# Optimization experiments

Measured on AMD Instinct MI355X. Metric: run time of the kernel, lower is better.

The kernel has to match this reference:

```python
import jax, jax.numpy as jnp
from jax import lax
import numpy as np

VOCAB, TAGS, EMB, HID = 50000, 45, 256, 512
B, S = 32, 256


def setup_inputs() -> dict:
    key = jax.random.key(0)
    ks = jax.random.split(key, 12)
    sc = 0.05
    return {
        "x": jax.random.randint(ks[0], (B, S), 0, VOCAB),
        "tags": jax.random.randint(ks[1], (B, S), 0, TAGS),
        "emb": jax.random.normal(ks[2], (VOCAB, EMB), jnp.float32) * sc,
        "w_ih_f": jax.random.normal(ks[3], (4 * HID, EMB), jnp.float32) * sc,
        "w_hh_f": jax.random.normal(ks[4], (4 * HID, HID), jnp.float32) * sc,
        "b_f": jnp.zeros((4 * HID,), jnp.float32),
        "w_ih_b": jax.random.normal(ks[5], (4 * HID, EMB), jnp.float32) * sc,
        "w_hh_b": jax.random.normal(ks[6], (4 * HID, HID), jnp.float32) * sc,
        "b_b": jnp.zeros((4 * HID,), jnp.float32),
        "lin_w": jax.random.normal(ks[7], (TAGS, 2 * HID), jnp.float32) * sc,
        "lin_b": jnp.zeros((TAGS,), jnp.float32),
        "start_t": jax.random.normal(ks[8], (TAGS,), jnp.float32) * 0.1,
        "end_t": jax.random.normal(ks[9], (TAGS,), jnp.float32) * 0.1,
        "trans": jax.random.normal(ks[10], (TAGS,), jnp.float32)[:, None] * 0.0 + jax.random.normal(ks[11], (TAGS, TAGS), jnp.float32) * 0.1,
    }


def _lstm_dir(xs, w_ih, w_hh, b, reverse):
    # xs: [B,S,E]. PyTorch gate order: i, f, g, o.
    Bsz = xs.shape[0]
    H = w_hh.shape[1]
    def step(carry, x_t):
        h, c = carry
        g = x_t @ w_ih.T + h @ w_hh.T + b
        i, f, gg, o = jnp.split(g, 4, axis=-1)
        c = jax.nn.sigmoid(f) * c + jax.nn.sigmoid(i) * jnp.tanh(gg)
        h = jax.nn.sigmoid(o) * jnp.tanh(c)
        return (h, c), h
    init = (jnp.zeros((Bsz, H), xs.dtype), jnp.zeros((Bsz, H), xs.dtype))
    _, hs = lax.scan(step, init, jnp.swapaxes(xs, 0, 1), reverse=reverse)
    return jnp.swapaxes(hs, 0, 1)  # [B,S,H]


def _crf_nll(em, tags, start_t, end_t, trans):
    # em: [B,S,T]; numerator: score of gold path
    em_sc = jnp.take_along_axis(em, tags[..., None], axis=2)[..., 0].sum(axis=1)
    tr_sc = trans[tags[:, :-1], tags[:, 1:]].sum(axis=1)
    score = start_t[tags[:, 0]] + em_sc + tr_sc + end_t[tags[:, -1]]
    # partition function via forward algorithm (logsumexp recurrence)
    alpha0 = start_t + em[:, 0]  # [B,T]
    def step(alpha, e_t):
        alpha = jax.nn.logsumexp(alpha[:, :, None] + trans[None], axis=1) + e_t
        return alpha, None
    alpha, _ = lax.scan(step, alpha0, jnp.swapaxes(em[:, 1:], 0, 1))
    logZ = jax.nn.logsumexp(alpha + end_t, axis=1)
    return -(score - logZ).mean()  # reduction='mean', loss = -llh


def reference(x, tags, emb, w_ih_f, w_hh_f, b_f, w_ih_b, w_hh_b, b_b,
              lin_w, lin_b, start_t, end_t, trans):
    embeds = emb[x]                               # [B,S,E]
    h_f = _lstm_dir(embeds, w_ih_f, w_hh_f, b_f, False)
    h_b = _lstm_dir(embeds, w_ih_b, w_hh_b, b_b, True)
    lstm_out = jnp.concatenate([h_f, h_b], axis=-1)  # [B,S,2H]
    emissions = lstm_out @ lin_w.T + lin_b           # [B,S,T]
    return _crf_nll(emissions, tags, start_t, end_t, trans)
```

## Files before the change

kernel.cpp:

```cpp
#include <hip/hip_runtime.h>

#define BB 32
#define SS 256
#define EMBD 256
#define HIDD 512
#define NTAG 45
#define TPAD 48
#define NBLK 32
#define ROWS 64
#define APAD 520
#define GRID_REC 256

typedef __bf16 bf16x8 __attribute__((ext_vector_type(8)));
typedef float  f32x4  __attribute__((ext_vector_type(4)));
typedef short  s16x8  __attribute__((ext_vector_type(8)));

__device__ __forceinline__ unsigned short f2bf(float x) {
  unsigned u = __builtin_bit_cast(unsigned, x);
  u = (u + 0x7fffu + ((u >> 16) & 1u)) >> 16;
  return (unsigned short)u;
}
__device__ __forceinline__ float bf2f(unsigned short u) {
  unsigned v = ((unsigned)u) << 16; return __builtin_bit_cast(float, v);
}

__device__ __forceinline__ unsigned ld32_cpol(const unsigned* p, bool sys) {
  unsigned v;
  if (sys) asm volatile("global_load_dword %0, %1, off sc0 sc1\ns_waitcnt vmcnt(0)"
                        : "=v"(v) : "v"(p) : "memory");
  else     asm volatile("global_load_dword %0, %1, off sc0\ns_waitcnt vmcnt(0)"
                        : "=v"(v) : "v"(p) : "memory");
  return v;
}
__device__ __forceinline__ void st32_cpol(unsigned* p, unsigned v, bool sys) {
  if (sys) asm volatile("global_store_dword %0, %1, off sc0 sc1" :: "v"(p), "v"(v) : "memory");
  else     asm volatile("global_store_dword %0, %1, off sc0"     :: "v"(p), "v"(v) : "memory");
}

#define LD8(CPOL)                                                           \
  asm volatile("global_load_dwordx4 %0, %[q0], off " CPOL "\n\t"            \
               "global_load_dwordx4 %1, %[q1], off " CPOL "\n\t"            \
               "global_load_dwordx4 %2, %[q2], off " CPOL "\n\t"            \
               "global_load_dwordx4 %3, %[q3], off " CPOL "\n\t"            \
               "global_load_dwordx4 %4, %[q4], off " CPOL "\n\t"            \
               "global_load_dwordx4 %5, %[q5], off " CPOL "\n\t"            \
               "global_load_dwordx4 %6, %[q6], off " CPOL "\n\t"            \
               "global_load_dwordx4 %7, %[q7], off " CPOL "\n\t"            \
               "s_waitcnt vmcnt(0)"                                         \
               : "=&v"(v0), "=&v"(v1), "=&v"(v2), "=&v"(v3),                \
                 "=&v"(v4), "=&v"(v5), "=&v"(v6), "=&v"(v7)                 \
               : [q0] "v"(p), [q1] "v"(p + 2048), [q2] "v"(p + 4096),       \
                 [q3] "v"(p + 6144), [q4] "v"(p + 8192), [q5] "v"(p + 10240),\
                 [q6] "v"(p + 12288), [q7] "v"(p + 14336)                   \
               : "memory")

__global__ void k_pack_e(const int* __restrict__ x, const float* __restrict__ emb,
                         unsigned short* __restrict__ E) {
  int idx = blockIdx.x * 256 + threadIdx.x;
  int e = idx & 255; int bt = idx >> 8; int b = bt & 31; int t = bt >> 5;
  int tok = x[b * SS + t];
  E[idx] = f2bf(emb[(long)tok * EMBD + e]);
}

__global__ void k_pack_w(const float* __restrict__ wih_f, const float* __restrict__ whh_f,
                         const float* __restrict__ bf_,  const float* __restrict__ wih_b,
                         const float* __restrict__ whh_b, const float* __restrict__ bb_,
                         unsigned short* __restrict__ Wh, unsigned short* __restrict__ Wie,
                         float* __restrict__ Bh) {
  long idx = (long)blockIdx.x * 256 + threadIdx.x;
  int k = (int)(idx % 768); long rest = idx / 768;
  int r2 = (int)(rest & 2047); int dir = (int)(rest >> 11);
  int blk = r2 >> 6, rl = r2 & 63, gate = rl >> 4, hl = rl & 15;
  int orig = gate * HIDD + blk * 16 + hl;
  const float* wih = dir ? wih_b : wih_f;
  const float* whh = dir ? whh_b : whh_f;
  if (k < HIDD) Wh[((long)(dir * 2048 + r2)) * 512 + k] = f2bf(whh[(long)orig * HIDD + k]);
  else          Wie[((long)(dir * 2048 + r2)) * 256 + (k - 512)] = f2bf(wih[(long)orig * EMBD + (k - 512)]);
  if (k == 0) {
    const float* bias = dir ? bb_ : bf_;
    Bh[dir * 2048 + r2] = bias[orig];
  }
}

__global__ void k_pack_l(const float* __restrict__ lin_w, const float* __restrict__ lin_b,
                         unsigned short* __restrict__ LW, float* __restrict__ LB) {
  int idx = blockIdx.x * 256 + threadIdx.x;
  if (idx < TPAD * 1024) {
    int tag = idx >> 10; int c = idx & 1023;
    LW[idx] = (tag < NTAG) ? f2bf(lin_w[tag * 1024 + c]) : (unsigned short)0;
  } else if (idx < TPAD * 1024 + TPAD) {
    int tag = idx - TPAD * 1024;
    LB[tag] = (tag < NTAG) ? lin_b[tag] : 0.f;
  }
}

__launch_bounds__(256)
__global__ void k_eproj(const unsigned short* __restrict__ E,
                        const unsigned short* __restrict__ Wie,
                        const float* __restrict__ Bh,
                        unsigned short* __restrict__ Ep) {
  __shared__ unsigned short W2[64 * 264];
  const int bx = blockIdx.x;
  const int tg = bx & 63, blk = (bx >> 6) & 31, dir = bx >> 11;
  const int tid = threadIdx.x;
  const int w = tid >> 6, lane = tid & 63;
  const int lm = lane & 15, quad = lane >> 4;

  {
    const unsigned short* src = Wie + ((long)(dir * 2048 + blk * 64)) * 256;
    for (int i = 0; i < 8; ++i) {
      int c = i * 256 + tid;
      int row = c >> 5, off = c & 31;
      *(s16x8*)&W2[row * 264 + off * 8] = *(const s16x8*)&src[row * 256 + off * 8];
    }
  }
  __syncthreads();

  f32x4 acc[2][4] = {};
#pragma unroll
  for (int kk = 0; kk < 8; ++kk) {
    s16x8 av[2];
#pragma unroll
    for (int sub = 0; sub < 2; ++sub)
      av[sub] = *(const s16x8*)&E[((long)(tg * 128 + w * 32 + sub * 16 + lm)) * 256 + kk * 32 + quad * 8];
#pragma unroll
    for (int sub = 0; sub < 2; ++sub)
#pragma unroll
      for (int n = 0; n < 4; ++n) {
        s16x8 bs = *(const s16x8*)&W2[(n * 16 + lm) * 264 + kk * 32 + quad * 8];
        acc[sub][n] = __builtin_amdgcn_mfma_f32_16x16x32_bf16(
            __builtin_bit_cast(bf16x8, av[sub]), __builtin_bit_cast(bf16x8, bs), acc[sub][n], 0, 0, 0);
      }
  }
  float bh[4];
#pragma unroll
  for (int n = 0; n < 4; ++n) bh[n] = Bh[dir * 2048 + blk * 64 + n * 16 + lm];
#pragma unroll
  for (int sub = 0; sub < 2; ++sub)
#pragma unroll
    for (int n = 0; n < 4; ++n)
#pragma unroll
      for (int r = 0; r < 4; ++r) {
        int m = w * 32 + sub * 16 + quad * 4 + r;
        int t = tg * 4 + (m >> 5), b = m & 31;
        int row_l = n * 16 + lm;
        Ep[((((long)(dir * 32 + blk) * 256 + t) * 32 + b) * 64) + row_l] =
            f2bf(acc[sub][n][r] + bh[n]);
      }
}

__launch_bounds__(256, 1)
__global__ void k_rec(const unsigned short* __restrict__ Wh,
                      const unsigned short* __restrict__ Ep,
                      unsigned short* __restrict__ H,
                      unsigned int* __restrict__ sync) {
  __shared__ unsigned short A_ls[32 * APAD];
  __shared__ float G_ls[32 * 66 + 4608];
  __shared__ int fast_ls;

  const int bx = blockIdx.x;
  const int role = bx & 7;
  if (role >= 2) return;
  const int dir = role;
  const int blk = bx >> 3;
  const int tid = threadIdx.x;
  const int w = tid >> 6, lane = tid & 63;
  const int lm = lane & 15, quad = lane >> 4;
  const int mt = w >> 1, nt = w & 1;

  unsigned int* det   = sync;
  unsigned int* flags = sync + 64;

  s16x8 wb[2][16];
  {
    const unsigned short* wsrc =
        Wh + ((long)(dir * 2048 + blk * 64 + nt * 32 + lm)) * 512 + quad * 8;
#pragma unroll
    for (int ns = 0; ns < 2; ++ns)
#pragma unroll
      for (int kk = 0; kk < 16; ++kk)
        wb[ns][kk] = *(const s16x8*)&wsrc[ns * 16 * 512 + kk * 32];
  }

  unsigned xcc;
  asm volatile("s_getreg_b32 %0, hwreg(HW_REG_XCC_ID)" : "=s"(xcc));
  if (tid == 0) st32_cpol(&det[dir * 32 + blk], xcc | 0x100u, true);
  if (w == 0) {
    unsigned v;
    for (;;) {
      v = (lane < 32) ? ld32_cpol(&det[dir * 32 + lane], true) : (xcc | 0x100u);
      if (__ballot(v != 0u) == ~0ull) break;
      __builtin_amdgcn_s_sleep(1);
    }
    if (lane == 0) fast_ls = (__ballot(v == (xcc | 0x100u)) == ~0ull) ? 1 : 0;
  }
  __syncthreads();
  const bool fast = (fast_ls != 0);
  __threadfence();

  const int gb = tid >> 3, hp = tid & 7;
  float c0 = 0.f, c1 = 0.f;

  unsigned short* Hd = H + (long)dir * SS * BB * HIDD;
  unsigned int* flagd = flags + dir * SS * NBLK;
  const unsigned short* Epd = Ep + ((long)(dir * 32 + blk) * 256) * 32 * 64;

  for (int t = 0; t < SS; ++t) {
    const int tE = (dir == 0) ? t : (SS - 1 - t);

    unsigned short epv[8];
    {
      const unsigned short* eb =
          Epd + ((long)tE * 32 + (mt * 16 + quad * 4)) * 64 + nt * 32 + lm;
#pragma unroll
      for (int ns = 0; ns < 2; ++ns)
#pragma unroll
        for (int r = 0; r < 4; ++r) epv[ns * 4 + r] = eb[r * 64 + ns * 16];
    }

    f32x4 acc0 = {0.f, 0.f, 0.f, 0.f}, acc1 = {0.f, 0.f, 0.f, 0.f};
    if (t > 0) {
      if (w == 0) {
        const unsigned int* fl = flagd + (long)(t - 1) * NBLK;
        for (;;) {
          unsigned f = (lane < 32) ? ld32_cpol(&fl[lane], !fast) : 1u;
          if (__ballot(f != 0u) == ~0ull) break;
          __builtin_amdgcn_s_sleep(1);
        }
      }
      __syncthreads();
      {
        const int hslot = (dir == 0) ? (t - 1) : (SS - t);
        const unsigned short* p = Hd + (long)hslot * BB * HIDD + w * 512 + lane * 8;
        s16x8 v0, v1, v2, v3, v4, v5, v6, v7;
        if (fast) { LD8("sc0"); } else { LD8("sc0 sc1"); }
        unsigned short* d = &A_ls[w * APAD + lane * 8];
        *(s16x8*)(d + 0 * 2080) = v0; *(s16x8*)(d + 1 * 2080) = v1;
        *(s16x8*)(d + 2 * 2080) = v2; *(s16x8*)(d + 3 * 2080) = v3;
        *(s16x8*)(d + 4 * 2080) = v4; *(s16x8*)(d + 5 * 2080) = v5;
        *(s16x8*)(d + 6 * 2080) = v6; *(s16x8*)(d + 7 * 2080) = v7;
      }
      __syncthreads();
#pragma unroll
      for (int kk = 0; kk < 16; ++kk) {
        s16x8 av = *(const s16x8*)&A_ls[(mt * 16 + lm) * APAD + kk * 32 + quad * 8];
        acc0 = __builtin_amdgcn_mfma_f32_16x16x32_bf16(
            __builtin_bit_cast(bf16x8, av), __builtin_bit_cast(bf16x8, wb[0][kk]), acc0, 0, 0, 0);
        acc1 = __builtin_amdgcn_mfma_f32_16x16x32_bf16(
            __builtin_bit_cast(bf16x8, av), __builtin_bit_cast(bf16x8, wb[1][kk]), acc1, 0, 0, 0);
      }
    }
#pragma unroll
    for (int r = 0; r < 4; ++r) {
      int mm = mt * 16 + quad * 4 + r;
      G_ls[mm * 66 + nt * 32 + lm]      = acc0[r] + bf2f(epv[r]);
      G_ls[mm * 66 + nt * 32 + 16 + lm] = acc1[r] + bf2f(epv[4 + r]);
    }
    __syncthreads();
    {
      float gi0 = G_ls[gb * 66 + 0  + 2 * hp], gi1 = G_ls[gb * 66 + 0  + 2 * hp + 1];
      float gf0 = G_ls[gb * 66 + 16 + 2 * hp], gf1 = G_ls[gb * 66 + 16 + 2 * hp + 1];
      float gg0 = G_ls[gb * 66 + 32 + 2 * hp], gg1 = G_ls[gb * 66 + 32 + 2 * hp + 1];
      float go0 = G_ls[gb * 66 + 48 + 2 * hp], go1 = G_ls[gb * 66 + 48 + 2 * hp + 1];
      float si0 = 1.f / (1.f + __expf(-gi0)), si1 = 1.f / (1.f + __expf(-gi1));
      float sf0 = 1.f / (1.f + __expf(-gf0)), sf1 = 1.f / (1.f + __expf(-gf1));
      float so0 = 1.f / (1.f + __expf(-go0)), so1 = 1.f / (1.f + __expf(-go1));
      float tg0 = tanhf(gg0), tg1 = tanhf(gg1);
      c0 = sf0 * c0 + si0 * tg0;
      c1 = sf1 * c1 + si1 * tg1;
      float h0 = so0 * tanhf(c0), h1 = so1 * tanhf(c1);
      int tslot = (dir == 0) ? t : (SS - 1 - t);
      unsigned hv = (unsigned)f2bf(h0) | ((unsigned)f2bf(h1) << 16);
      st32_cpol((unsigned*)&Hd[(long)tslot * BB * HIDD + (long)gb * HIDD + blk * 16 + 2 * hp],
                hv, !fast);
    }
    __syncthreads();
    if (t < SS - 1 && tid == 0)
      st32_cpol(&flagd[(long)t * NBLK + blk], 1u, !fast);
  }
}

__launch_bounds__(256)
__global__ void k_emis(const unsigned short* __restrict__ H,
                       const unsigned short* __restrict__ LW,
                       const float* __restrict__ LB,
                       float* __restrict__ EM) {
  const int row0 = blockIdx.x * 32;
  const int tid = threadIdx.x;
  const int w = tid >> 6, lane = tid & 63;
  const int lm = lane & 15, quad = lane >> 4;
  const unsigned short* Hf = H;
  const unsigned short* Hb = H + (long)SS * BB * HIDD;

  for (int tile = w; tile < 6; tile += 4) {
    int mt = tile / 3, nt = tile % 3;
    int arow = row0 + mt * 16 + lm;
    int nrow = nt * 16 + lm;
    f32x4 acc = {0.f, 0.f, 0.f, 0.f};
#pragma unroll 4
    for (int kk = 0; kk < 32; ++kk) {
      int k0 = kk * 32 + quad * 8;
      s16x8 asv = (k0 < HIDD) ? *(const s16x8*)&Hf[(long)arow * HIDD + k0]
                              : *(const s16x8*)&Hb[(long)arow * HIDD + (k0 - HIDD)];
      s16x8 bsv = *(const s16x8*)&LW[nrow * 1024 + k0];
      acc = __builtin_amdgcn_mfma_f32_16x16x32_bf16(
          __builtin_bit_cast(bf16x8, asv), __builtin_bit_cast(bf16x8, bsv), acc, 0, 0, 0);
    }
    float bias = LB[nrow];
#pragma unroll
    for (int r = 0; r < 4; ++r) {
      int mm = row0 + mt * 16 + quad * 4 + r;
      EM[(long)mm * TPAD + nrow] = acc[r] + bias;
    }
  }
}

__global__ void k_crf(const int* __restrict__ tags, const float* __restrict__ start_t,
                      const float* __restrict__ end_t, const float* __restrict__ trans,
                      const float* __restrict__ EM, float* __restrict__ chain) {
  __shared__ float T_ls[NTAG * TPAD];
  __shared__ float ET[48 * 48 + 16];
  __shared__ float P_ls[64];
  const int b = blockIdx.x;
  const int lane = threadIdx.x;
  const int j = lane;

  for (int i = lane; i < NTAG * NTAG; i += 64)
    T_ls[(i / NTAG) * TPAD + (i % NTAG)] = trans[i];
  for (int i = lane; i < 48 * 48 + 16; i += 64) ET[i] = 0.f;
  __syncthreads();

  float Mj = -1e30f;
  if (j < NTAG) {
    for (int i = 0; i < NTAG; ++i) Mj = fmaxf(Mj, T_ls[i * TPAD + j]);
    for (int i = 0; i < NTAG; ++i) ET[i * 48 + j] = __expf(T_ls[i * TPAD + j] - Mj);
  }
  __syncthreads();

  float et[48];
#pragma unroll
  for (int i = 0; i < 48; ++i) et[i] = ET[i * 48 + j];

  float part = 0.f;
  for (int t = lane; t < SS; t += 64) {
    int tg = tags[b * SS + t];
    part += EM[((long)t * BB + b) * TPAD + tg];
    if (t + 1 < SS) part += T_ls[tg * TPAD + tags[b * SS + t + 1]];
    if (t == 0)      part += start_t[tg];
    if (t == SS - 1) part += end_t[tg];
  }
  for (int off = 32; off; off >>= 1) part += __shfl_down(part, off);
  float score = __shfl(part, 0);

  float alpha = (j < NTAG) ? (start_t[j] + EM[(long)b * TPAD + j]) : -1e30f;
  float e_next = (j < NTAG) ? EM[((long)BB + b) * TPAD + j] : 0.f;
  for (int t = 1; t < SS; ++t) {
    float e_cur = e_next;
    if (t < SS - 1) e_next = (j < NTAG) ? EM[((long)(t + 1) * BB + b) * TPAD + j] : 0.f;
    float am = alpha;
#pragma unroll
    for (int off = 32; off; off >>= 1) am = fmaxf(am, __shfl_xor(am, off));
    float p = __expf(alpha - am);
    P_ls[lane] = p;
    __builtin_amdgcn_wave_barrier();
    float s0 = 0.f, s1 = 0.f, s2 = 0.f, s3 = 0.f;
#pragma unroll
    for (int i0 = 0; i0 < 48; i0 += 4) {
      f32x4 pv = *(const f32x4*)&P_ls[i0];
      s0 += pv.x * et[i0];
      s1 += pv.y * et[i0 + 1];
      s2 += pv.z * et[i0 + 2];
      s3 += pv.w * et[i0 + 3];
    }
    __builtin_amdgcn_wave_barrier();
    float s = (s0 + s1) + (s2 + s3);
    float na = am + Mj + __logf(s) + e_cur;
    alpha = (j < NTAG) ? na : -1e30f;
  }
  float v = (j < NTAG) ? (alpha + end_t[j]) : -1e30f;
  float mx = v;
  for (int off = 32; off; off >>= 1) mx = fmaxf(mx, __shfl_xor(mx, off));
  float s = __expf(v - mx);
  for (int off = 32; off; off >>= 1) s += __shfl_xor(s, off);
  if (lane == 0) chain[b] = score - (mx + __logf(s));
}

__global__ void k_fin(const float* __restrict__ chain, float* __restrict__ out) {
  int lane = threadIdx.x;
  float v = (lane < BB) ? chain[lane] : 0.f;
  for (int off = 32; off; off >>= 1) v += __shfl_xor(v, off);
  if (lane == 0) out[0] = -v / (float)BB;
}

extern "C" void kernel_launch(void* const* d_in, const int* in_sizes, int n_in,
                              void* d_out, int out_size, void* d_ws, size_t ws_size,
                              hipStream_t stream) {
  const int*   x      = (const int*)d_in[0];
  const int*   tags   = (const int*)d_in[1];
  const float* emb    = (const float*)d_in[2];
  const float* wih_f  = (const float*)d_in[3];
  const float* whh_f  = (const float*)d_in[4];
  const float* b_f    = (const float*)d_in[5];
  const float* wih_b  = (const float*)d_in[6];
  const float* whh_b  = (const float*)d_in[7];
  const float* b_b    = (const float*)d_in[8];
  const float* lin_w  = (const float*)d_in[9];
  const float* lin_b  = (const float*)d_in[10];
  const float* start_t= (const float*)d_in[11];
  const float* end_t  = (const float*)d_in[12];
  const float* trans  = (const float*)d_in[13];

  char* ws = (char*)d_ws;
  size_t off = 0;
  auto alloc = [&](size_t bytes) {
    void* p = ws + off; off = (off + bytes + 255) & ~(size_t)255; return p;
  };
  size_t sync_bytes = (64 + 2 * SS * NBLK) * 4;
  unsigned int*   sync = (unsigned int*) alloc(sync_bytes);
  unsigned short* E   = (unsigned short*)alloc((size_t)SS * BB * EMBD * 2);
  unsigned short* Wh  = (unsigned short*)alloc((size_t)2 * 2048 * 512 * 2);
  unsigned short* Wie = (unsigned short*)alloc((size_t)2 * 2048 * 256 * 2);
  float*          Bh  = (float*)         alloc((size_t)2 * 2048 * 4);
  unsigned short* Ep  = (unsigned short*)alloc((size_t)2 * 32 * 256 * 32 * 64 * 2);
  unsigned short* H   = (unsigned short*)alloc((size_t)2 * SS * BB * HIDD * 2);
  unsigned short* LW  = (unsigned short*)alloc((size_t)TPAD * 1024 * 2);
  float*          LB  = (float*)         alloc((size_t)TPAD * 4);
  float*          EM  = (float*)         alloc((size_t)SS * BB * TPAD * 4);
  float*          chain = (float*)       alloc((size_t)BB * 4);

  hipMemsetAsync(sync, 0, sync_bytes, stream);
  k_pack_e<<<dim3((SS * BB * EMBD) / 256), dim3(256), 0, stream>>>(x, emb, E);
  k_pack_w<<<dim3((2 * 2048 * 768) / 256), dim3(256), 0, stream>>>(
      wih_f, whh_f, b_f, wih_b, whh_b, b_b, Wh, Wie, Bh);
  k_pack_l<<<dim3((TPAD * 1024 + TPAD + 255) / 256), dim3(256), 0, stream>>>(
      lin_w, lin_b, LW, LB);
  k_eproj<<<dim3(4096), dim3(256), 0, stream>>>(E, Wie, Bh, Ep);

  void* kargs[] = {&Wh, &Ep, &H, &sync};
  hipLaunchCooperativeKernel((const void*)k_rec, dim3(GRID_REC), dim3(256), kargs, 0, stream);

  k_emis<<<dim3((SS * BB) / 32), dim3(256), 0, stream>>>(H, LW, LB, EM);
  k_crf<<<dim3(BB), dim3(64), 0, stream>>>(tags, start_t, end_t, trans, EM, chain);
  k_fin<<<dim3(1), dim3(64), 0, stream>>>(chain, (float*)d_out);
}
```

Before: 1.073 ms.

## Replace per-step flag barriers with sentinel-polled hidden-state data in LSTM recurrence

The recurrent kernel no longer publishes per-block flags and waits on them each timestep. The H buffer is pre-filled with a sentinel byte pattern, and each consumer re-reads the previous hidden state with system-coherent loads until no sentinel words remain. This removes a barrier, a flag store and a flag poll from the serial critical path. The grid also shrinks to exactly the 64 working blocks, and the same-XCC detection fast path is dropped, so every access now uses system-scope cache policy. The trade-offs are a memset of the whole H buffer, and the risk that a genuine bf16 pair equal to the sentinel value would cause an endless spin.

```diff
diff --git a/kernel.cpp b/kernel.cpp
--- a/kernel.cpp
+++ b/kernel.cpp
@@ -7,13 +7,14 @@
 #define NTAG 45
 #define TPAD 48
 #define NBLK 32
-#define ROWS 64
 #define APAD 520
-#define GRID_REC 256
+#define GRID_REC 64
+#define SENT 0x01010101u
 
 typedef __bf16 bf16x8 __attribute__((ext_vector_type(8)));
 typedef float  f32x4  __attribute__((ext_vector_type(4)));
 typedef short  s16x8  __attribute__((ext_vector_type(8)));
+typedef unsigned u32x4 __attribute__((ext_vector_type(4)));
 
 __device__ __forceinline__ unsigned short f2bf(float x) {
   unsigned u = __builtin_bit_cast(unsigned, x);
@@ -24,17 +25,8 @@
   unsigned v = ((unsigned)u) << 16; return __builtin_bit_cast(float, v);
 }
 
-__device__ __forceinline__ unsigned ld32_cpol(const unsigned* p, bool sys) {
-  unsigned v;
-  if (sys) asm volatile("global_load_dword %0, %1, off sc0 sc1\ns_waitcnt vmcnt(0)"
-                        : "=v"(v) : "v"(p) : "memory");
-  else     asm volatile("global_load_dword %0, %1, off sc0\ns_waitcnt vmcnt(0)"
-                        : "=v"(v) : "v"(p) : "memory");
-  return v;
-}
-__device__ __forceinline__ void st32_cpol(unsigned* p, unsigned v, bool sys) {
-  if (sys) asm volatile("global_store_dword %0, %1, off sc0 sc1" :: "v"(p), "v"(v) : "memory");
-  else     asm volatile("global_store_dword %0, %1, off sc0"     :: "v"(p), "v"(v) : "memory");
+__device__ __forceinline__ void st32_sys(unsigned* p, unsigned v) {
+  asm volatile("global_store_dword %0, %1, off sc0 sc1" :: "v"(p), "v"(v) : "memory");
 }
 
 #define LD8(CPOL)                                                           \
@@ -152,25 +144,18 @@
 __launch_bounds__(256, 1)
 __global__ void k_rec(const unsigned short* __restrict__ Wh,
                       const unsigned short* __restrict__ Ep,
-                      unsigned short* __restrict__ H,
-                      unsigned int* __restrict__ sync) {
+                      unsigned short* __restrict__ H) {
   __shared__ unsigned short A_ls[32 * APAD];
-  __shared__ float G_ls[32 * 66 + 4608];
-  __shared__ int fast_ls;
+  __shared__ float G_ls[32 * 66];
 
   const int bx = blockIdx.x;
-  const int role = bx & 7;
-  if (role >= 2) return;
-  const int dir = role;
-  const int blk = bx >> 3;
+  const int dir = bx & 1;
+  const int blk = bx >> 1;
   const int tid = threadIdx.x;
   const int w = tid >> 6, lane = tid & 63;
   const int lm = lane & 15, quad = lane >> 4;
   const int mt = w >> 1, nt = w & 1;
 
-  unsigned int* det   = sync;
-  unsigned int* flags = sync + 64;
-
   s16x8 wb[2][16];
   {
     const unsigned short* wsrc =
@@ -182,27 +167,10 @@
         wb[ns][kk] = *(const s16x8*)&wsrc[ns * 16 * 512 + kk * 32];
   }
 
-  unsigned xcc;
-  asm volatile("s_getreg_b32 %0, hwreg(HW_REG_XCC_ID)" : "=s"(xcc));
-  if (tid == 0) st32_cpol(&det[dir * 32 + blk], xcc | 0x100u, true);
-  if (w == 0) {
-    unsigned v;
-    for (;;) {
-      v = (lane < 32) ? ld32_cpol(&det[dir * 32 + lane], true) : (xcc | 0x100u);
-      if (__ballot(v != 0u) == ~0ull) break;
-      __builtin_amdgcn_s_sleep(1);
-    }
-    if (lane == 0) fast_ls = (__ballot(v == (xcc | 0x100u)) == ~0ull) ? 1 : 0;
-  }
-  __syncthreads();
-  const bool fast = (fast_ls != 0);
-  __threadfence();
-
   const int gb = tid >> 3, hp = tid & 7;
-  float c0 = 0.f, c1 = 0.f;
+  float c0s = 0.f, c1s = 0.f;
 
   unsigned short* Hd = H + (long)dir * SS * BB * HIDD;
-  unsigned int* flagd = flags + dir * SS * NBLK;
   const unsigned short* Epd = Ep + ((long)(dir * 32 + blk) * 256) * 32 * 64;
 
   for (int t = 0; t < SS; ++t) {
@@ -220,20 +188,27 @@
 
     f32x4 acc0 = {0.f, 0.f, 0.f, 0.f}, acc1 = {0.f, 0.f, 0.f, 0.f};
     if (t > 0) {
-      if (w == 0) {
-        const unsigned int* fl = flagd + (long)(t - 1) * NBLK;
-        for (;;) {
-          unsigned f = (lane < 32) ? ld32_cpol(&fl[lane], !fast) : 1u;
-          if (__ballot(f != 0u) == ~0ull) break;
-          __builtin_amdgcn_s_sleep(1);
-        }
-      }
-      __syncthreads();
       {
         const int hslot = (dir == 0) ? (t - 1) : (SS - t);
         const unsigned short* p = Hd + (long)hslot * BB * HIDD + w * 512 + lane * 8;
         s16x8 v0, v1, v2, v3, v4, v5, v6, v7;
-        if (fast) { LD8("sc0"); } else { LD8("sc0 sc1"); }
+        unsigned bad;
+        do {
+          LD8("sc0 sc1");
+          u32x4 u0 = __builtin_bit_cast(u32x4, v0), u1 = __builtin_bit_cast(u32x4, v1);
+          u32x4 u2 = __builtin_bit_cast(u32x4, v2), u3 = __builtin_bit_cast(u32x4, v3);
+          u32x4 u4 = __builtin_bit_cast(u32x4, v4), u5 = __builtin_bit_cast(u32x4, v5);
+          u32x4 u6 = __builtin_bit_cast(u32x4, v6), u7 = __builtin_bit_cast(u32x4, v7);
+          unsigned b0 = (u0.x == SENT) | (u0.y == SENT) | (u0.z == SENT) | (u0.w == SENT);
+          unsigned b1 = (u1.x == SENT) | (u1.y == SENT) | (u1.z == SENT) | (u1.w == SENT);
+          unsigned b2 = (u2.x == SENT) | (u2.y == SENT) | (u2.z == SENT) | (u2.w == SENT);
+          unsigned b3 = (u3.x == SENT) | (u3.y == SENT) | (u3.z == SENT) | (u3.w == SENT);
+          unsigned b4 = (u4.x == SENT) | (u4.y == SENT) | (u4.z == SENT) | (u4.w == SENT);
+          unsigned b5 = (u5.x == SENT) | (u5.y == SENT) | (u5.z == SENT) | (u5.w == SENT);
+          unsigned b6 = (u6.x == SENT) | (u6.y == SENT) | (u6.z == SENT) | (u6.w == SENT);
+          unsigned b7 = (u7.x == SENT) | (u7.y == SENT) | (u7.z == SENT) | (u7.w == SENT);
+          bad = (b0 | b1) | (b2 | b3) | ((b4 | b5) | (b6 | b7));
+        } while (__builtin_expect(bad != 0u, 0));
         unsigned short* d = &A_ls[w * APAD + lane * 8];
         *(s16x8*)(d + 0 * 2080) = v0; *(s16x8*)(d + 1 * 2080) = v1;
         *(s16x8*)(d + 2 * 2080) = v2; *(s16x8*)(d + 3 * 2080) = v3;
@@ -266,17 +241,13 @@
       float sf0 = 1.f / (1.f + __expf(-gf0)), sf1 = 1.f / (1.f + __expf(-gf1));
       float so0 = 1.f / (1.f + __expf(-go0)), so1 = 1.f / (1.f + __expf(-go1));
       float tg0 = tanhf(gg0), tg1 = tanhf(gg1);
-      c0 = sf0 * c0 + si0 * tg0;
-      c1 = sf1 * c1 + si1 * tg1;
-      float h0 = so0 * tanhf(c0), h1 = so1 * tanhf(c1);
+      c0s = sf0 * c0s + si0 * tg0;
+      c1s = sf1 * c1s + si1 * tg1;
+      float h0 = so0 * tanhf(c0s), h1 = so1 * tanhf(c1s);
       int tslot = (dir == 0) ? t : (SS - 1 - t);
       unsigned hv = (unsigned)f2bf(h0) | ((unsigned)f2bf(h1) << 16);
-      st32_cpol((unsigned*)&Hd[(long)tslot * BB * HIDD + (long)gb * HIDD + blk * 16 + 2 * hp],
-                hv, !fast);
-    }
-    __syncthreads();
-    if (t < SS - 1 && tid == 0)
-      st32_cpol(&flagd[(long)t * NBLK + blk], 1u, !fast);
+      st32_sys((unsigned*)&Hd[(long)tslot * BB * HIDD + (long)gb * HIDD + blk * 16 + 2 * hp], hv);
+    }
   }
 }
 
@@ -415,8 +386,6 @@
   auto alloc = [&](size_t bytes) {
     void* p = ws + off; off = (off + bytes + 255) & ~(size_t)255; return p;
   };
-  size_t sync_bytes = (64 + 2 * SS * NBLK) * 4;
-  unsigned int*   sync = (unsigned int*) alloc(sync_bytes);
   unsigned short* E   = (unsigned short*)alloc((size_t)SS * BB * EMBD * 2);
   unsigned short* Wh  = (unsigned short*)alloc((size_t)2 * 2048 * 512 * 2);
   unsigned short* Wie = (unsigned short*)alloc((size_t)2 * 2048 * 256 * 2);
@@ -428,7 +397,7 @@
   float*          EM  = (float*)         alloc((size_t)SS * BB * TPAD * 4);
   float*          chain = (float*)       alloc((size_t)BB * 4);
 
-  hipMemsetAsync(sync, 0, sync_bytes, stream);
+  hipMemsetAsync(H, 0x01, (size_t)2 * SS * BB * HIDD * 2, stream);
   k_pack_e<<<dim3((SS * BB * EMBD) / 256), dim3(256), 0, stream>>>(x, emb, E);
   k_pack_w<<<dim3((2 * 2048 * 768) / 256), dim3(256), 0, stream>>>(
       wih_f, whh_f, b_f, wih_b, whh_b, b_b, Wh, Wie, Bh);
@@ -436,7 +405,7 @@
       lin_w, lin_b, LW, LB);
   k_eproj<<<dim3(4096), dim3(256), 0, stream>>>(E, Wie, Bh, Ep);
 
-  void* kargs[] = {&Wh, &Ep, &H, &sync};
+  void* kargs[] = {&Wh, &Ep, &H};
   hipLaunchCooperativeKernel((const void*)k_rec, dim3(GRID_REC), dim3(256), kargs, 0, stream);
 
   k_emis<<<dim3((SS * BB) / 32), dim3(256), 0, stream>>>(H, LW, LB, EM);
```

Result: slower. 1.105 ms (+3.0%).
